# Performance work log

Measured on AMD Instinct MI355X. Metric: run time of the kernel, lower is better.

Reference implementation:

```python
import jax, jax.numpy as jnp
import numpy as np

T, B, IN, H, OUT = 345, 128, 13, 128, 9

# snnTorch ATan surrogate spike: forward = heaviside(x), backward = 1/(1+(pi*x)^2) (alpha=2)
@jax.custom_vjp
def spike_fn(x):
    return (x > 0).astype(x.dtype)

def _spike_fwd(x):
    return spike_fn(x), x

def _spike_bwd(x, g):
    return (g / (1.0 + (jnp.pi * x) ** 2),)

spike_fn.defvjp(_spike_fwd, _spike_bwd)


def setup_inputs() -> dict:
    key = jax.random.key(0)
    ks = jax.random.split(key, 5)
    x = jax.random.normal(ks[0], (B, IN, T), dtype=jnp.float32)
    # PyTorch Linear init: U(-1/sqrt(fan_in), 1/sqrt(fan_in))
    lim1 = 1.0 / np.sqrt(IN)
    lim2 = 1.0 / np.sqrt(H)
    W1 = jax.random.uniform(ks[1], (H, IN), minval=-lim1, maxval=lim1, dtype=jnp.float32)
    b1 = jax.random.uniform(ks[2], (H,), minval=-lim1, maxval=lim1, dtype=jnp.float32)
    W2 = jax.random.uniform(ks[3], (OUT, H), minval=-lim2, maxval=lim2, dtype=jnp.float32)
    b2 = jax.random.uniform(ks[4], (OUT,), minval=-lim2, maxval=lim2, dtype=jnp.float32)
    beta1 = jnp.float32(0.9)
    thr1 = jnp.float32(1.0)
    beta2 = jnp.float32(0.9)
    thr2 = jnp.float32(1.0)
    return {"x": x, "W1": W1, "b1": b1, "W2": W2, "b2": b2,
            "beta1": beta1, "thr1": thr1, "beta2": beta2, "thr2": thr2}


def reference(x, W1, b1, W2, b2, beta1, thr1, beta2, thr2):
    # Precompute fc1 for all steps: (T, B, H)
    cur1_all = jnp.einsum('bct,hc->tbh', x, W1) + b1
    bt1 = jnp.clip(beta1, 0.0, 1.0)
    bt2 = jnp.clip(beta2, 0.0, 1.0)

    def step(carry, cur1):
        mem1, mem2 = carry
        mem1 = bt1 * mem1 + cur1                 # leaky integrate
        spk1 = spike_fn(mem1 - thr1)             # fire
        mem1 = mem1 - spk1 * thr1                # subtract reset
        cur2 = spk1 @ W2.T + b2                  # (B, OUT)
        mem2 = bt2 * mem2 + cur2
        spk2 = spike_fn(mem2 - thr2)
        mem2 = mem2 - spk2 * thr2
        return (mem1, mem2), (spk2, mem2)

    init = (jnp.zeros((B, H), x.dtype), jnp.zeros((B, OUT), x.dtype))
    _, (spk_rec, mem_rec) = jax.lax.scan(step, init, cur1_all)
    return spk_rec, mem_rec  # each (T, B, OUT)
```

## Files before the change

### kernel.cpp

```cpp
#include <hip/hip_runtime.h>

#define T_STEPS 345
#define B_SZ    128
#define IN_SZ   13
#define H_SZ    128
#define OUT_SZ  9
#define XPITCH  16
#define TPAD    384
#define NBO     (B_SZ * OUT_SZ)
#define MASK_BYTES (B_SZ * T_STEPS * 2 * 8)

__global__ __launch_bounds__(128, 1)
void k1_spikes(const float* __restrict__ x, const float* __restrict__ W1,
               const float* __restrict__ b1, const float* __restrict__ beta1p,
               const float* __restrict__ thr1p,
               unsigned long long* __restrict__ masks)
{
    const int b   = blockIdx.x;
    const int tid = threadIdx.x;

    __shared__ float xst[(T_STEPS + 3) * XPITCH];

    const float* xb = x + (size_t)b * (IN_SZ * T_STEPS);
    for (int i = tid; i < IN_SZ * T_STEPS; i += 128) {
        const int c = i / T_STEPS;
        const int t = i - c * T_STEPS;
        xst[t * XPITCH + c] = xb[i];
    }

    const float bt1 = fminf(fmaxf(beta1p[0], 0.0f), 1.0f);
    const float th1 = thr1p[0];

    float w1r[IN_SZ];
#pragma unroll
    for (int c = 0; c < IN_SZ; ++c) w1r[c] = W1[tid * IN_SZ + c];
    const float b1r = b1[tid];

    float mem1 = 0.0f;
    unsigned long long* mp = masks + (size_t)b * (T_STEPS * 2) + (tid >> 6);
    const bool store_lane = (tid & 63) == 0;

    __syncthreads();

    const float4* xq = (const float4*)xst;
    float4 a0 = xq[0], a1 = xq[1], a2 = xq[2]; float a3 = xst[12];
    float4 c0 = xq[4], c1 = xq[5], c2 = xq[6]; float c3 = xst[XPITCH + 12];

    int t = 0;
    for (; t < T_STEPS - 1; t += 2) {
        const float xa[IN_SZ] = { a0.x,a0.y,a0.z,a0.w, a1.x,a1.y,a1.z,a1.w,
                                  a2.x,a2.y,a2.z,a2.w, a3 };
        const float xc[IN_SZ] = { c0.x,c0.y,c0.z,c0.w, c1.x,c1.y,c1.z,c1.w,
                                  c2.x,c2.y,c2.z,c2.w, c3 };
        a0 = xq[(t+2)*4+0]; a1 = xq[(t+2)*4+1]; a2 = xq[(t+2)*4+2]; a3 = xst[(t+2)*XPITCH+12];
        c0 = xq[(t+3)*4+0]; c1 = xq[(t+3)*4+1]; c2 = xq[(t+3)*4+2]; c3 = xst[(t+3)*XPITCH+12];

        float cura = b1r, curb = b1r;
#pragma unroll
        for (int c = 0; c < IN_SZ; ++c) {
            cura = fmaf(xa[c], w1r[c], cura);
            curb = fmaf(xc[c], w1r[c], curb);
        }

        mem1 = fmaf(bt1, mem1, cura);
        const bool pa = mem1 > th1;
        const unsigned long long ma = __ballot(pa);
        mem1 = fmaf(pa ? -1.0f : 0.0f, th1, mem1);
        if (store_lane) mp[0] = ma;

        mem1 = fmaf(bt1, mem1, curb);
        const bool pb = mem1 > th1;
        const unsigned long long mb = __ballot(pb);
        mem1 = fmaf(pb ? -1.0f : 0.0f, th1, mem1);
        if (store_lane) mp[2] = mb;

        mp += 4;
    }
    {
        const float xa[IN_SZ] = { a0.x,a0.y,a0.z,a0.w, a1.x,a1.y,a1.z,a1.w,
                                  a2.x,a2.y,a2.z,a2.w, a3 };
        float cura = b1r;
#pragma unroll
        for (int c = 0; c < IN_SZ; ++c) cura = fmaf(xa[c], w1r[c], cura);
        mem1 = fmaf(bt1, mem1, cura);
        const bool pa = mem1 > th1;
        const unsigned long long ma = __ballot(pa);
        if (store_lane) mp[0] = ma;
    }
}

__global__ __launch_bounds__(256, 1)
void k2_gemm(const unsigned long long* __restrict__ masks,
             const float* __restrict__ W2, const float* __restrict__ b2,
             float* __restrict__ cur2)
{
    const int gw   = blockIdx.x * 4 + (threadIdx.x >> 6);
    const int lane = threadIdx.x & 63;
    const int bo   = gw / 6;
    const int w    = gw - bo * 6;
    const int b    = bo / 9;
    const int o    = bo - b * 9;
    const int t    = w * 64 + lane;
    const int tc   = (t < T_STEPS) ? t : (T_STEPS - 1);

    const uint4 mm = *(const uint4*)((const char*)masks +
                                     ((size_t)b * T_STEPS + tc) * 16);

    const float* __restrict__ w2row = W2 + o * H_SZ;
    float acc = 0.0f;
#pragma unroll
    for (int h = 0; h < 32; ++h)
        acc = fmaf((float)((mm.x >> h) & 1u), w2row[h], acc);
#pragma unroll
    for (int h = 0; h < 32; ++h)
        acc = fmaf((float)((mm.y >> h) & 1u), w2row[32 + h], acc);
#pragma unroll
    for (int h = 0; h < 32; ++h)
        acc = fmaf((float)((mm.z >> h) & 1u), w2row[64 + h], acc);
#pragma unroll
    for (int h = 0; h < 32; ++h)
        acc = fmaf((float)((mm.w >> h) & 1u), w2row[96 + h], acc);

    cur2[(size_t)bo * TPAD + t] = acc + b2[o];
}

__global__ __launch_bounds__(64, 1)
void k3_scan2(const float* __restrict__ cur2, const float* __restrict__ beta2p,
              const float* __restrict__ thr2p, float* __restrict__ out)
{
    const int lid = blockIdx.x * 64 + threadIdx.x;
    const float bt2 = fminf(fmaxf(beta2p[0], 0.0f), 1.0f);
    const float th2 = thr2p[0];

    const float4* __restrict__ src = (const float4*)(cur2 + (size_t)lid * TPAD);
    float* __restrict__ out_spk = out + lid;
    float* __restrict__ out_mem = out + (size_t)T_STEPS * NBO + lid;

    float mem2 = 0.0f;

    float4 f0 = src[0], f1 = src[1], f2 = src[2], f3 = src[3];

    for (int g = 0; g < 88; g += 4) {
        const float4 u0 = f0, u1 = f1, u2 = f2, u3 = f3;
        f0 = src[g + 4]; f1 = src[g + 5]; f2 = src[g + 6]; f3 = src[g + 7];

        const float4 us[4] = { u0, u1, u2, u3 };
#pragma unroll
        for (int j = 0; j < 4; ++j) {
            const float vv[4] = { us[j].x, us[j].y, us[j].z, us[j].w };
#pragma unroll
            for (int k = 0; k < 4; ++k) {
                const int tt = (g + j) * 4 + k;
                mem2 = fmaf(bt2, mem2, vv[k]);
                const float s2 = (mem2 > th2) ? 1.0f : 0.0f;
                mem2 = fmaf(-s2, th2, mem2);
                if (tt < T_STEPS) {
                    out_spk[(size_t)tt * NBO] = s2;
                    out_mem[(size_t)tt * NBO] = mem2;
                }
            }
        }
    }
}

extern "C" void kernel_launch(void* const* d_in, const int* in_sizes, int n_in,
                              void* d_out, int out_size, void* d_ws, size_t ws_size,
                              hipStream_t stream) {
    const float* x     = (const float*)d_in[0];
    const float* W1    = (const float*)d_in[1];
    const float* b1    = (const float*)d_in[2];
    const float* W2    = (const float*)d_in[3];
    const float* b2    = (const float*)d_in[4];
    const float* beta1 = (const float*)d_in[5];
    const float* thr1  = (const float*)d_in[6];
    const float* beta2 = (const float*)d_in[7];
    const float* thr2  = (const float*)d_in[8];
    float* out = (float*)d_out;

    char* ws = (char*)d_ws;
    unsigned long long* masks = (unsigned long long*)ws;
    float* cur2 = (float*)(ws + MASK_BYTES);

    k1_spikes<<<dim3(B_SZ), dim3(128), 0, stream>>>(x, W1, b1, beta1, thr1, masks);
    k2_gemm  <<<dim3(1728), dim3(256), 0, stream>>>(masks, W2, b2, cur2);
    k3_scan2 <<<dim3(NBO / 64), dim3(64), 0, stream>>>(cur2, beta2, thr2, out);
}
```

Before: 125.1 us.

## Fuse spike scan, W2 matmul and output scan into one kernel via shared memory

```diff
diff --git a/kernel.cpp b/kernel.cpp
--- a/kernel.cpp
+++ b/kernel.cpp
@@ -7,156 +7,161 @@
 #define OUT_SZ  9
 #define XPITCH  16
 #define TPAD    384
+#define CPAD    388
 #define NBO     (B_SZ * OUT_SZ)
-#define MASK_BYTES (B_SZ * T_STEPS * 2 * 8)
 
-__global__ __launch_bounds__(128, 1)
-void k1_spikes(const float* __restrict__ x, const float* __restrict__ W1,
-               const float* __restrict__ b1, const float* __restrict__ beta1p,
-               const float* __restrict__ thr1p,
-               unsigned long long* __restrict__ masks)
+__global__ __launch_bounds__(512, 2)
+void snn_fused(const float* __restrict__ x, const float* __restrict__ W1,
+               const float* __restrict__ b1, const float* __restrict__ W2,
+               const float* __restrict__ b2,
+               const float* __restrict__ beta1p, const float* __restrict__ thr1p,
+               const float* __restrict__ beta2p, const float* __restrict__ thr2p,
+               float* __restrict__ out)
 {
-    const int b   = blockIdx.x;
-    const int tid = threadIdx.x;
+    const int b    = blockIdx.x >> 1;
+    const int half = blockIdx.x & 1;
+    const int tid  = threadIdx.x;
 
     __shared__ float xst[(T_STEPS + 3) * XPITCH];
+    __shared__ unsigned long long msh[TPAD * 2];
+    __shared__ float c2s[OUT_SZ * CPAD];
 
     const float* xb = x + (size_t)b * (IN_SZ * T_STEPS);
-    for (int i = tid; i < IN_SZ * T_STEPS; i += 128) {
+    for (int i = tid; i < IN_SZ * T_STEPS; i += 512) {
         const int c = i / T_STEPS;
         const int t = i - c * T_STEPS;
         xst[t * XPITCH + c] = xb[i];
     }
-
-    const float bt1 = fminf(fmaxf(beta1p[0], 0.0f), 1.0f);
-    const float th1 = thr1p[0];
-
-    float w1r[IN_SZ];
-#pragma unroll
-    for (int c = 0; c < IN_SZ; ++c) w1r[c] = W1[tid * IN_SZ + c];
-    const float b1r = b1[tid];
-
-    float mem1 = 0.0f;
-    unsigned long long* mp = masks + (size_t)b * (T_STEPS * 2) + (tid >> 6);
-    const bool store_lane = (tid & 63) == 0;
-
     __syncthreads();
 
-    const float4* xq = (const float4*)xst;
-    float4 a0 = xq[0], a1 = xq[1], a2 = xq[2]; float a3 = xst[12];
-    float4 c0 = xq[4], c1 = xq[5], c2 = xq[6]; float c3 = xst[XPITCH + 12];
+    if (tid < 128) {
+        const float bt1 = fminf(fmaxf(beta1p[0], 0.0f), 1.0f);
+        const float th1 = thr1p[0];
 
-    int t = 0;
-    for (; t < T_STEPS - 1; t += 2) {
-        const float xa[IN_SZ] = { a0.x,a0.y,a0.z,a0.w, a1.x,a1.y,a1.z,a1.w,
-                                  a2.x,a2.y,a2.z,a2.w, a3 };
-        const float xc[IN_SZ] = { c0.x,c0.y,c0.z,c0.w, c1.x,c1.y,c1.z,c1.w,
-                                  c2.x,c2.y,c2.z,c2.w, c3 };
-        a0 = xq[(t+2)*4+0]; a1 = xq[(t+2)*4+1]; a2 = xq[(t+2)*4+2]; a3 = xst[(t+2)*XPITCH+12];
-        c0 = xq[(t+3)*4+0]; c1 = xq[(t+3)*4+1]; c2 = xq[(t+3)*4+2]; c3 = xst[(t+3)*XPITCH+12];
+        float w1r[IN_SZ];
+#pragma unroll
+        for (int c = 0; c < IN_SZ; ++c) w1r[c] = W1[tid * IN_SZ + c];
+        const float b1r = b1[tid];
 
-        float cura = b1r, curb = b1r;
+        float mem1 = 0.0f;
+        unsigned long long* mp = msh + (tid >> 6);
+        const bool store_lane = (tid & 63) == 0;
+
+        const float4* xq = (const float4*)xst;
+        float4 a0 = xq[0], a1 = xq[1], a2 = xq[2]; float a3 = xst[12];
+        float4 c0 = xq[4], c1 = xq[5], c2 = xq[6]; float c3 = xst[XPITCH + 12];
+
+        int t = 0;
+        for (; t < T_STEPS - 1; t += 2) {
+            const float xa[IN_SZ] = { a0.x,a0.y,a0.z,a0.w, a1.x,a1.y,a1.z,a1.w,
+                                      a2.x,a2.y,a2.z,a2.w, a3 };
+            const float xc[IN_SZ] = { c0.x,c0.y,c0.z,c0.w, c1.x,c1.y,c1.z,c1.w,
+                                      c2.x,c2.y,c2.z,c2.w, c3 };
+            a0 = xq[(t+2)*4+0]; a1 = xq[(t+2)*4+1]; a2 = xq[(t+2)*4+2]; a3 = xst[(t+2)*XPITCH+12];
+            c0 = xq[(t+3)*4+0]; c1 = xq[(t+3)*4+1]; c2 = xq[(t+3)*4+2]; c3 = xst[(t+3)*XPITCH+12];
+
+            float cura = b1r, curb = b1r;
 #pragma unroll
-        for (int c = 0; c < IN_SZ; ++c) {
-            cura = fmaf(xa[c], w1r[c], cura);
-            curb = fmaf(xc[c], w1r[c], curb);
+            for (int c = 0; c < IN_SZ; ++c) {
+                cura = fmaf(xa[c], w1r[c], cura);
+                curb = fmaf(xc[c], w1r[c], curb);
+            }
+
+            mem1 = fmaf(bt1, mem1, cura);
+            const bool pa = mem1 > th1;
+            const unsigned long long ma = __ballot(pa);
+            mem1 = fmaf(pa ? -1.0f : 0.0f, th1, mem1);
+            if (store_lane) mp[0] = ma;
+
+            mem1 = fmaf(bt1, mem1, curb);
+            const bool pb = mem1 > th1;
+            const unsigned long long mb = __ballot(pb);
+            mem1 = fmaf(pb ? -1.0f : 0.0f, th1, mem1);
+            if (store_lane) mp[2] = mb;
+
+            mp += 4;
         }
+        {
+            const float xa[IN_SZ] = { a0.x,a0.y,a0.z,a0.w, a1.x,a1.y,a1.z,a1.w,
+                                      a2.x,a2.y,a2.z,a2.w, a3 };
+            float cura = b1r;
+#pragma unroll
+            for (int c = 0; c < IN_SZ; ++c) cura = fmaf(xa[c], w1r[c], cura);
+            mem1 = fmaf(bt1, mem1, cura);
+            const bool pa = mem1 > th1;
+            const unsigned long long ma = __ballot(pa);
+            if (store_lane) mp[0] = ma;
+        }
+    }
+    __syncthreads();
 
-        mem1 = fmaf(bt1, mem1, cura);
-        const bool pa = mem1 > th1;
-        const unsigned long long ma = __ballot(pa);
-        mem1 = fmaf(pa ? -1.0f : 0.0f, th1, mem1);
-        if (store_lane) mp[0] = ma;
+    {
+        const int wave = tid >> 6;
+        const int lane = tid & 63;
+        const int tstart = half ? 30 : 0;
+        const int tend   = half ? 54 : 30;
+        for (int task = tstart + wave; task < tend; task += 8) {
+            const int o  = task / 6;
+            const int w  = task - o * 6;
+            const int t  = w * 64 + lane;
+            const int tc = (t < T_STEPS) ? t : (T_STEPS - 1);
 
-        mem1 = fmaf(bt1, mem1, curb);
-        const bool pb = mem1 > th1;
-        const unsigned long long mb = __ballot(pb);
-        mem1 = fmaf(pb ? -1.0f : 0.0f, th1, mem1);
-        if (store_lane) mp[2] = mb;
+            const uint4 mm = *(const uint4*)((const char*)msh + (size_t)tc * 16);
 
-        mp += 4;
+            const float* __restrict__ w2row = W2 + o * H_SZ;
+            float acc = 0.0f;
+#pragma unroll
+            for (int h = 0; h < 32; ++h)
+                acc = fmaf((float)((mm.x >> h) & 1u), w2row[h], acc);
+#pragma unroll
+            for (int h = 0; h < 32; ++h)
+                acc = fmaf((float)((mm.y >> h) & 1u), w2row[32 + h], acc);
+#pragma unroll
+            for (int h = 0; h < 32; ++h)
+                acc = fmaf((float)((mm.z >> h) & 1u), w2row[64 + h], acc);
+#pragma unroll
+            for (int h = 0; h < 32; ++h)
+                acc = fmaf((float)((mm.w >> h) & 1u), w2row[96 + h], acc);
+
+            c2s[o * CPAD + t] = acc + b2[o];
+        }
     }
+    __syncthreads();
+
     {
-        const float xa[IN_SZ] = { a0.x,a0.y,a0.z,a0.w, a1.x,a1.y,a1.z,a1.w,
-                                  a2.x,a2.y,a2.z,a2.w, a3 };
-        float cura = b1r;
+        const int nrows = half ? 4 : 5;
+        if (tid < nrows) {
+            const int o = (half ? 5 : 0) + tid;
+            const float bt2 = fminf(fmaxf(beta2p[0], 0.0f), 1.0f);
+            const float th2 = thr2p[0];
+            const int lid = b * OUT_SZ + o;
+
+            const float4* __restrict__ src = (const float4*)(c2s + o * CPAD);
+            float* __restrict__ out_spk = out + lid;
+            float* __restrict__ out_mem = out + (size_t)T_STEPS * NBO + lid;
+
+            float mem2 = 0.0f;
+            float4 f0 = src[0], f1 = src[1], f2 = src[2], f3 = src[3];
+
+            for (int g = 0; g < 88; g += 4) {
+                const float4 u0 = f0, u1 = f1, u2 = f2, u3 = f3;
+                f0 = src[g + 4]; f1 = src[g + 5]; f2 = src[g + 6]; f3 = src[g + 7];
+
+                const float4 us[4] = { u0, u1, u2, u3 };
 #pragma unroll
-        for (int c = 0; c < IN_SZ; ++c) cura = fmaf(xa[c], w1r[c], cura);
-        mem1 = fmaf(bt1, mem1, cura);
-        const bool pa = mem1 > th1;
-        const unsigned long long ma = __ballot(pa);
-        if (store_lane) mp[0] = ma;
-    }
-}
-
-__global__ __launch_bounds__(256, 1)
-void k2_gemm(const unsigned long long* __restrict__ masks,
-             const float* __restrict__ W2, const float* __restrict__ b2,
-             float* __restrict__ cur2)
-{
-    const int gw   = blockIdx.x * 4 + (threadIdx.x >> 6);
-    const int lane = threadIdx.x & 63;
-    const int bo   = gw / 6;
-    const int w    = gw - bo * 6;
-    const int b    = bo / 9;
-    const int o    = bo - b * 9;
-    const int t    = w * 64 + lane;
-    const int tc   = (t < T_STEPS) ? t : (T_STEPS - 1);
-
-    const uint4 mm = *(const uint4*)((const char*)masks +
-                                     ((size_t)b * T_STEPS + tc) * 16);
-
-    const float* __restrict__ w2row = W2 + o * H_SZ;
-    float acc = 0.0f;
+                for (int j = 0; j < 4; ++j) {
+                    const float vv[4] = { us[j].x, us[j].y, us[j].z, us[j].w };
 #pragma unroll
-    for (int h = 0; h < 32; ++h)
-        acc = fmaf((float)((mm.x >> h) & 1u), w2row[h], acc);
-#pragma unroll
-    for (int h = 0; h < 32; ++h)
-        acc = fmaf((float)((mm.y >> h) & 1u), w2row[32 + h], acc);
-#pragma unroll
-    for (int h = 0; h < 32; ++h)
-        acc = fmaf((float)((mm.z >> h) & 1u), w2row[64 + h], acc);
-#pragma unroll
-    for (int h = 0; h < 32; ++h)
-        acc = fmaf((float)((mm.w >> h) & 1u), w2row[96 + h], acc);
-
-    cur2[(size_t)bo * TPAD + t] = acc + b2[o];
-}
-
-__global__ __launch_bounds__(64, 1)
-void k3_scan2(const float* __restrict__ cur2, const float* __restrict__ beta2p,
-              const float* __restrict__ thr2p, float* __restrict__ out)
-{
-    const int lid = blockIdx.x * 64 + threadIdx.x;
-    const float bt2 = fminf(fmaxf(beta2p[0], 0.0f), 1.0f);
-    const float th2 = thr2p[0];
-
-    const float4* __restrict__ src = (const float4*)(cur2 + (size_t)lid * TPAD);
-    float* __restrict__ out_spk = out + lid;
-    float* __restrict__ out_mem = out + (size_t)T_STEPS * NBO + lid;
-
-    float mem2 = 0.0f;
-
-    float4 f0 = src[0], f1 = src[1], f2 = src[2], f3 = src[3];
-
-    for (int g = 0; g < 88; g += 4) {
-        const float4 u0 = f0, u1 = f1, u2 = f2, u3 = f3;
-        f0 = src[g + 4]; f1 = src[g + 5]; f2 = src[g + 6]; f3 = src[g + 7];
-
-        const float4 us[4] = { u0, u1, u2, u3 };
-#pragma unroll
-        for (int j = 0; j < 4; ++j) {
-            const float vv[4] = { us[j].x, us[j].y, us[j].z, us[j].w };
-#pragma unroll
-            for (int k = 0; k < 4; ++k) {
-                const int tt = (g + j) * 4 + k;
-                mem2 = fmaf(bt2, mem2, vv[k]);
-                const float s2 = (mem2 > th2) ? 1.0f : 0.0f;
-                mem2 = fmaf(-s2, th2, mem2);
-                if (tt < T_STEPS) {
-                    out_spk[(size_t)tt * NBO] = s2;
-                    out_mem[(size_t)tt * NBO] = mem2;
+                    for (int k = 0; k < 4; ++k) {
+                        const int tt = (g + j) * 4 + k;
+                        mem2 = fmaf(bt2, mem2, vv[k]);
+                        const float s2 = (mem2 > th2) ? 1.0f : 0.0f;
+                        mem2 = fmaf(-s2, th2, mem2);
+                        if (tt < T_STEPS) {
+                            out_spk[(size_t)tt * NBO] = s2;
+                            out_mem[(size_t)tt * NBO] = mem2;
+                        }
+                    }
                 }
             }
         }
@@ -176,12 +181,8 @@
     const float* beta2 = (const float*)d_in[7];
     const float* thr2  = (const float*)d_in[8];
     float* out = (float*)d_out;
+    (void)in_sizes; (void)n_in; (void)out_size; (void)d_ws; (void)ws_size;
 
-    char* ws = (char*)d_ws;
-    unsigned long long* masks = (unsigned long long*)ws;
-    float* cur2 = (float*)(ws + MASK_BYTES);
-
-    k1_spikes<<<dim3(B_SZ), dim3(128), 0, stream>>>(x, W1, b1, beta1, thr1, masks);
-    k2_gemm  <<<dim3(1728), dim3(256), 0, stream>>>(masks, W2, b2, cur2);
-    k3_scan2 <<<dim3(NBO / 64), dim3(64), 0, stream>>>(cur2, beta2, thr2, out);
+    snn_fused<<<dim3(B_SZ * 2), dim3(512), 0, stream>>>(
+        x, W1, b1, W2, b2, beta1, thr1, beta2, thr2, out);
 }
```

New measurement: 123.9 us. Within noise of the previous version (-1.0%).
